# Kernel tuning notes

Measured on AMD Instinct MI355X. Metric: run time of the kernel, lower is better.

Reference implementation:

```python
import jax, jax.numpy as jnp
import numpy as np

B, S, N, H, V = 8, 512, 32, 256, 100001
NEG = -1e9
SLOPE = 0.2  # LeakyReLU negative slope


def setup_inputs() -> dict:
    key = jax.random.key(0)
    k1, k2, k3, k4, k5 = jax.random.split(key, 5)
    node_ids = jax.random.randint(k1, (B, S), 0, V)
    neighs = jax.random.randint(k2, (B, S, N), 0, V)
    mask = jax.random.randint(k3, (B, S, N, 1), 0, 2).astype(jnp.int32)
    emb_table = jax.random.normal(k4, (V, H), dtype=jnp.float32) * 0.02
    a_w = jax.random.normal(k5, (2 * H, 1), dtype=jnp.float32) * (1.0 / np.sqrt(2 * H))
    a_b = jnp.zeros((1,), dtype=jnp.float32)
    return {"node_ids": node_ids, "neighs": neighs, "mask": mask,
            "emb_table": emb_table, "a_w": a_w, "a_b": a_b}


def reference(node_ids, neighs, mask, emb_table, a_w, a_b):
    # Gather embeddings
    src = emb_table[node_ids][:, :, None, :]          # [B,S,1,H]
    nbr = emb_table[neighs]                           # [B,S,N,H]
    neigh_embs = jnp.concatenate([src, nbr], axis=2)  # [B,S,N+1,H] (self + neighbors)
    # Concat src with each candidate -> [B,S,N+1,2H]
    src_rep = jnp.broadcast_to(src, neigh_embs.shape)
    embs = jnp.concatenate([src_rep, neigh_embs], axis=-1)
    # Tiny linear (2H -> 1) + LeakyReLU(0.2)
    z = embs @ a_w + a_b                              # [B,S,N+1,1]
    att = jnp.where(z > 0, z, SLOPE * z)
    # Mask neighbor slots (self at index 0 is never masked)
    att = att.at[:, :, 1:].add(mask.astype(att.dtype) * NEG)
    w = jax.nn.softmax(att, axis=2)                   # [B,S,N+1,1]
    # Weighted aggregate: w^T @ neigh_embs
    out = jnp.sum(w * neigh_embs, axis=2)             # [B,S,H]
    return out
```

## Files before the change

kernel.cpp:

```cpp
#include <hip/hip_runtime.h>
#include <math.h>


constexpr int   H     = 256;
constexpr int   NN    = 32;
constexpr int   C     = NN + 1;
constexpr float SLOPE = 0.2f;

constexpr int RPI = 4;

__global__ __launch_bounds__(256) void proj_kernel(
    const float* __restrict__ emb,
    const float* __restrict__ a_w,
    float2*      __restrict__ pv,
    int V)
{
  const int lane = threadIdx.x & 63;
  const int wid  = blockIdx.x * 4 + (threadIdx.x >> 6);
  const int nw   = gridDim.x * 4;
  const int l4   = lane << 2;

  const float4 aw1 = *(const float4*)(a_w + l4);
  const float4 aw2 = *(const float4*)(a_w + H + l4);
  const float4* __restrict__ embv = (const float4*)emb;

  for (int base = wid * RPI; base < V; base += nw * RPI) {
    float red[2 * RPI];
#pragma unroll
    for (int i = 0; i < RPI; ++i) {
      float4 r = {0.f, 0.f, 0.f, 0.f};
      if (base + i < V) r = embv[(size_t)(base + i) * (H / 4) + lane];
      red[2 * i]     = r.x * aw1.x + r.y * aw1.y + r.z * aw1.z + r.w * aw1.w;
      red[2 * i + 1] = r.x * aw2.x + r.y * aw2.y + r.z * aw2.z + r.w * aw2.w;
    }
#pragma unroll
    for (int off = 32; off > 0; off >>= 1)
#pragma unroll
      for (int t = 0; t < 2 * RPI; ++t)
        red[t] += __shfl_xor(red[t], off, 64);
    if (lane == 0) {
#pragma unroll
      for (int i = 0; i < RPI; ++i)
        if (base + i < V)
          pv[base + i] = make_float2(red[2 * i], red[2 * i + 1]);
    }
  }
}

__global__ __launch_bounds__(256) void agg_kernel(
    const int*    __restrict__ node_ids,
    const int*    __restrict__ neighs,
    const int*    __restrict__ mask,
    const float*  __restrict__ emb,
    const float2* __restrict__ pv,
    const float*  __restrict__ a_b,
    float*        __restrict__ out,
    int npos)
{
  __shared__ int sidx[4][64];
  const int wv   = threadIdx.x >> 6;
  const int lane = threadIdx.x & 63;
  const int pos  = blockIdx.x * 4 + wv;
  if (pos >= npos) return;
  const int l4 = lane << 2;

  bool active = false;
  int  my     = 0;
  if (lane == 0) {
    my = node_ids[pos];
    active = true;
  } else if (lane <= NN) {
    my     = neighs[pos * NN + lane - 1];
    active = (mask[pos * NN + lane - 1] == 0);
  }
  const unsigned long long bal = __ballot(active);
  const int K = (int)__popcll(bal);
  if (active)
    sidx[wv][(int)__popcll(bal & ((1ull << lane) - 1ull))] = my;
  const int cidx = sidx[wv][lane];

  const float4* __restrict__ embv = (const float4*)emb;

  constexpr int PF = 8;
  float4 buf[PF];
#pragma unroll
  for (int j = 0; j < PF; ++j)
    if (j < K)
      buf[j] = embv[(size_t)__builtin_amdgcn_readlane(cidx, j) * (H / 4) + lane];

  const int   iself = __builtin_amdgcn_readlane(cidx, 0);
  const float psrc  = pv[iself].x;
  const float ab    = a_b[0];
  float z = -1e30f;
  if (lane < K) {
    const float zc = psrc + pv[cidx].y + ab;
    z = (zc > 0.f) ? zc : SLOPE * zc;
  }
  float m = z;
#pragma unroll
  for (int off = 32; off > 0; off >>= 1)
    m = fmaxf(m, __shfl_xor(m, off, 64));
  float pr = (lane < K) ? __expf(z - m) : 0.f;
  float s = pr;
#pragma unroll
  for (int off = 32; off > 0; off >>= 1)
    s += __shfl_xor(s, off, 64);
  const float inv = 1.f / s;

  float4 acc0 = {0.f, 0.f, 0.f, 0.f};
  float4 acc1 = {0.f, 0.f, 0.f, 0.f};
#pragma unroll
  for (int c = 0; c < C; ++c) {
    if (c < K) {
      const float wc = __int_as_float(
          __builtin_amdgcn_readlane(__float_as_int(pr), c));
      float4 r;
      if (c < PF) r = buf[c];
      else        r = embv[(size_t)__builtin_amdgcn_readlane(cidx, c) * (H / 4) + lane];
      if (c & 1) {
        acc1.x += wc * r.x; acc1.y += wc * r.y;
        acc1.z += wc * r.z; acc1.w += wc * r.w;
      } else {
        acc0.x += wc * r.x; acc0.y += wc * r.y;
        acc0.z += wc * r.z; acc0.w += wc * r.w;
      }
    }
  }
  float4 o;
  o.x = (acc0.x + acc1.x) * inv;
  o.y = (acc0.y + acc1.y) * inv;
  o.z = (acc0.z + acc1.z) * inv;
  o.w = (acc0.w + acc1.w) * inv;
  *(float4*)(out + (size_t)pos * H + l4) = o;
}

extern "C" void kernel_launch(void* const* d_in, const int* in_sizes, int n_in,
                              void* d_out, int out_size, void* d_ws, size_t ws_size,
                              hipStream_t stream) {
  const int*   node_ids = (const int*)d_in[0];
  const int*   neighs   = (const int*)d_in[1];
  const int*   mask     = (const int*)d_in[2];
  const float* emb      = (const float*)d_in[3];
  const float* a_w      = (const float*)d_in[4];
  const float* a_b      = (const float*)d_in[5];
  float*       out      = (float*)d_out;

  const int npos = in_sizes[0];
  const int V    = in_sizes[3] / H;

  float2* pv = (float2*)d_ws;

  proj_kernel<<<2048, 256, 0, stream>>>(emb, a_w, pv, V);
  agg_kernel<<<(npos + 3) / 4, 256, 0, stream>>>(node_ids, neighs, mask, emb,
                                                 pv, a_b, out, npos);
}
```

Before: 176.4 us.

## Fuse projection into aggregation and split candidates across two wavefronts per position

Drops the separate pass that projected the whole embedding table (about 100k rows) through the attention weights. Each position now computes attention scores on the fly from the rows it gathers anyway. Each position is handled by two wavefronts that take alternating candidates and keep all gathered rows in registers. Their partial online-softmax states are merged through shared memory. This removes a full-table read, at the cost of redundant dot products, extra shuffle reductions and a block-level sync.

```diff
diff --git a/kernel.cpp b/kernel.cpp
--- a/kernel.cpp
+++ b/kernel.cpp
@@ -5,64 +5,27 @@
 constexpr int   H     = 256;
 constexpr int   NN    = 32;
 constexpr int   C     = NN + 1;
+constexpr int   JMAX  = (C + 1) / 2;
 constexpr float SLOPE = 0.2f;
 
-constexpr int RPI = 4;
-
-__global__ __launch_bounds__(256) void proj_kernel(
+__global__ __launch_bounds__(256, 4) void gat_kernel(
+    const int*   __restrict__ node_ids,
+    const int*   __restrict__ neighs,
+    const int*   __restrict__ mask,
     const float* __restrict__ emb,
     const float* __restrict__ a_w,
-    float2*      __restrict__ pv,
-    int V)
+    const float* __restrict__ a_b,
+    float*       __restrict__ out)
 {
-  const int lane = threadIdx.x & 63;
-  const int wid  = blockIdx.x * 4 + (threadIdx.x >> 6);
-  const int nw   = gridDim.x * 4;
-  const int l4   = lane << 2;
+  __shared__ int    sidx[4][64];
+  __shared__ float4 sacc[4][64];
+  __shared__ float  sm[4], ss[4];
 
-  const float4 aw1 = *(const float4*)(a_w + l4);
-  const float4 aw2 = *(const float4*)(a_w + H + l4);
-  const float4* __restrict__ embv = (const float4*)emb;
-
-  for (int base = wid * RPI; base < V; base += nw * RPI) {
-    float red[2 * RPI];
-#pragma unroll
-    for (int i = 0; i < RPI; ++i) {
-      float4 r = {0.f, 0.f, 0.f, 0.f};
-      if (base + i < V) r = embv[(size_t)(base + i) * (H / 4) + lane];
-      red[2 * i]     = r.x * aw1.x + r.y * aw1.y + r.z * aw1.z + r.w * aw1.w;
-      red[2 * i + 1] = r.x * aw2.x + r.y * aw2.y + r.z * aw2.z + r.w * aw2.w;
-    }
-#pragma unroll
-    for (int off = 32; off > 0; off >>= 1)
-#pragma unroll
-      for (int t = 0; t < 2 * RPI; ++t)
-        red[t] += __shfl_xor(red[t], off, 64);
-    if (lane == 0) {
-#pragma unroll
-      for (int i = 0; i < RPI; ++i)
-        if (base + i < V)
-          pv[base + i] = make_float2(red[2 * i], red[2 * i + 1]);
-    }
-  }
-}
-
-__global__ __launch_bounds__(256) void agg_kernel(
-    const int*    __restrict__ node_ids,
-    const int*    __restrict__ neighs,
-    const int*    __restrict__ mask,
-    const float*  __restrict__ emb,
-    const float2* __restrict__ pv,
-    const float*  __restrict__ a_b,
-    float*        __restrict__ out,
-    int npos)
-{
-  __shared__ int sidx[4][64];
   const int wv   = threadIdx.x >> 6;
   const int lane = threadIdx.x & 63;
-  const int pos  = blockIdx.x * 4 + wv;
-  if (pos >= npos) return;
-  const int l4 = lane << 2;
+  const int pos  = blockIdx.x * 2 + (wv >> 1);
+  const int half = wv & 1;
+  const int l4   = lane << 2;
 
   bool active = false;
   int  my     = 0;
@@ -80,58 +43,81 @@
   const int cidx = sidx[wv][lane];
 
   const float4* __restrict__ embv = (const float4*)emb;
+  const int iself = __builtin_amdgcn_readlane(cidx, 0);
 
-  constexpr int PF = 8;
-  float4 buf[PF];
+  const float4 rs = embv[(size_t)iself * (H / 4) + lane];
+  float4 buf[JMAX];
 #pragma unroll
-  for (int j = 0; j < PF; ++j)
-    if (j < K)
-      buf[j] = embv[(size_t)__builtin_amdgcn_readlane(cidx, j) * (H / 4) + lane];
+  for (int j = 0; j < JMAX; ++j) {
+    const int c = half + 2 * j;
+    if (c < K) {
+      const int ic = __builtin_amdgcn_readlane(cidx, c);
+      buf[j] = embv[(size_t)ic * (H / 4) + lane];
+    }
+  }
 
-  const int   iself = __builtin_amdgcn_readlane(cidx, 0);
-  const float psrc  = pv[iself].x;
-  const float ab    = a_b[0];
-  float z = -1e30f;
-  if (lane < K) {
-    const float zc = psrc + pv[cidx].y + ab;
-    z = (zc > 0.f) ? zc : SLOPE * zc;
+  const float4 aw1 = *(const float4*)(a_w + l4);
+  const float4 aw2 = *(const float4*)(a_w + H + l4);
+  const float  ab  = a_b[0];
+
+  float red[JMAX + 1];
+  red[0] = rs.x * aw1.x + rs.y * aw1.y + rs.z * aw1.z + rs.w * aw1.w;
+#pragma unroll
+  for (int j = 0; j < JMAX; ++j) {
+    const int c = half + 2 * j;
+    red[j + 1] = 0.f;
+    if (c < K)
+      red[j + 1] = buf[j].x * aw2.x + buf[j].y * aw2.y +
+                   buf[j].z * aw2.z + buf[j].w * aw2.w;
   }
-  float m = z;
 #pragma unroll
   for (int off = 32; off > 0; off >>= 1)
-    m = fmaxf(m, __shfl_xor(m, off, 64));
-  float pr = (lane < K) ? __expf(z - m) : 0.f;
-  float s = pr;
 #pragma unroll
-  for (int off = 32; off > 0; off >>= 1)
-    s += __shfl_xor(s, off, 64);
-  const float inv = 1.f / s;
+    for (int t = 0; t <= JMAX; ++t)
+      red[t] += __shfl_xor(red[t], off, 64);
+  const float zsrc = red[0];
 
-  float4 acc0 = {0.f, 0.f, 0.f, 0.f};
-  float4 acc1 = {0.f, 0.f, 0.f, 0.f};
+  float m = -1e30f;
 #pragma unroll
-  for (int c = 0; c < C; ++c) {
+  for (int j = 0; j < JMAX; ++j) {
+    const int c = half + 2 * j;
     if (c < K) {
-      const float wc = __int_as_float(
-          __builtin_amdgcn_readlane(__float_as_int(pr), c));
-      float4 r;
-      if (c < PF) r = buf[c];
-      else        r = embv[(size_t)__builtin_amdgcn_readlane(cidx, c) * (H / 4) + lane];
-      if (c & 1) {
-        acc1.x += wc * r.x; acc1.y += wc * r.y;
-        acc1.z += wc * r.z; acc1.w += wc * r.w;
-      } else {
-        acc0.x += wc * r.x; acc0.y += wc * r.y;
-        acc0.z += wc * r.z; acc0.w += wc * r.w;
-      }
+      const float z = zsrc + red[j + 1] + ab;
+      red[j + 1] = (z > 0.f) ? z : SLOPE * z;
+      m = fmaxf(m, red[j + 1]);
     }
   }
-  float4 o;
-  o.x = (acc0.x + acc1.x) * inv;
-  o.y = (acc0.y + acc1.y) * inv;
-  o.z = (acc0.z + acc1.z) * inv;
-  o.w = (acc0.w + acc1.w) * inv;
-  *(float4*)(out + (size_t)pos * H + l4) = o;
+  float  s   = 0.f;
+  float4 acc = {0.f, 0.f, 0.f, 0.f};
+#pragma unroll
+  for (int j = 0; j < JMAX; ++j) {
+    const int c = half + 2 * j;
+    if (c < K) {
+      const float pr = __expf(red[j + 1] - m);
+      s += pr;
+      acc.x += pr * buf[j].x; acc.y += pr * buf[j].y;
+      acc.z += pr * buf[j].z; acc.w += pr * buf[j].w;
+    }
+  }
+
+  sacc[wv][lane] = acc;
+  if (lane == 0) { sm[wv] = m; ss[wv] = s; }
+  __syncthreads();
+
+  if (half == 0) {
+    const float  m1 = sm[wv + 1], s1 = ss[wv + 1];
+    const float  M  = fmaxf(m, m1);
+    const float  f0 = __expf(m - M);
+    const float  f1 = __expf(m1 - M);
+    const float4 a1 = sacc[wv + 1][lane];
+    const float  inv = 1.f / (f0 * s + f1 * s1);
+    float4 o;
+    o.x = (f0 * acc.x + f1 * a1.x) * inv;
+    o.y = (f0 * acc.y + f1 * a1.y) * inv;
+    o.z = (f0 * acc.z + f1 * a1.z) * inv;
+    o.w = (f0 * acc.w + f1 * a1.w) * inv;
+    *(float4*)(out + (size_t)pos * H + l4) = o;
+  }
 }
 
 extern "C" void kernel_launch(void* const* d_in, const int* in_sizes, int n_in,
@@ -146,11 +132,6 @@
   float*       out      = (float*)d_out;
 
   const int npos = in_sizes[0];
-  const int V    = in_sizes[3] / H;
-
-  float2* pv = (float2*)d_ws;
-
-  proj_kernel<<<2048, 256, 0, stream>>>(emb, a_w, pv, V);
-  agg_kernel<<<(npos + 3) / 4, 256, 0, stream>>>(node_ids, neighs, mask, emb,
-                                                 pv, a_b, out, npos);
+  gat_kernel<<<npos / 2, 256, 0, stream>>>(node_ids, neighs, mask, emb,
+                                           a_w, a_b, out);
 }
```

New measurement: 155.8 us. 1.13x faster.
